# Kernel tuning notes

Hardware: AMD Instinct MI355X
Metric: run time of the kernel (lower is better)

The kernel has to match this reference:

```python
import jax, jax.numpy as jnp
import numpy as np

B, S, V, E, H, L = 64, 512, 32000, 512, 1024, 2


def setup_inputs() -> dict:
    key = jax.random.key(0)
    ks = jax.random.split(key, 12)
    sc = 0.05
    x = jax.random.randint(ks[0], (B, S), 0, V)
    emb = jax.random.normal(ks[1], (V, E), dtype=jnp.float32) * sc
    # Gate weights stacked along output dim in order [f, i, g, o] -> [4H, in_dim]
    Wx0 = jax.random.normal(ks[2], (4 * H, E), dtype=jnp.float32) * sc
    bx0 = jnp.zeros((4 * H,), dtype=jnp.float32)
    Wh0 = jax.random.normal(ks[3], (4 * H, H), dtype=jnp.float32) * sc
    bh0 = jnp.zeros((4 * H,), dtype=jnp.float32)
    Wx1 = jax.random.normal(ks[4], (4 * H, H), dtype=jnp.float32) * sc
    bx1 = jnp.zeros((4 * H,), dtype=jnp.float32)
    Wh1 = jax.random.normal(ks[5], (4 * H, H), dtype=jnp.float32) * sc
    bh1 = jnp.zeros((4 * H,), dtype=jnp.float32)
    fc_w = jax.random.normal(ks[6], (1, H), dtype=jnp.float32) * sc
    fc_b = jnp.zeros((1,), dtype=jnp.float32)
    return {"x": x, "emb": emb, "Wx0": Wx0, "bx0": bx0, "Wh0": Wh0, "bh0": bh0,
            "Wx1": Wx1, "bx1": bx1, "Wh1": Wh1, "bh1": bh1,
            "fc_w": fc_w, "fc_b": fc_b}


def _lstm_cell(inp, h, c, Wx, bx, Wh, bh):
    # Fused 4-gate GEMM, then split: order [forget, input, candidate, output]
    z = inp @ Wx.T + bx + h @ Wh.T + bh            # [B, 4H]
    f, i, g, o = jnp.split(z, 4, axis=-1)
    f = jax.nn.sigmoid(f)
    i = jax.nn.sigmoid(i)
    g = jnp.tanh(g)
    o = jax.nn.sigmoid(o)
    c = f * c + i * g
    h = o * jnp.tanh(c)
    return h, c


def reference(x, emb, Wx0, bx0, Wh0, bh0, Wx1, bx1, Wh1, bh1, fc_w, fc_b):
    xe = emb[x]                                     # [B, S, E]
    xts = jnp.swapaxes(xe, 0, 1)                    # [S, B, E] for scan
    b = xe.shape[0]
    zeros = jnp.zeros((b, H), dtype=xe.dtype)
    carry0 = (zeros, zeros, zeros, zeros)           # h0, c0, h1, c1

    def step(carry, xt):
        h0, c0, h1, c1 = carry
        h0, c0 = _lstm_cell(xt, h0, c0, Wx0, bx0, Wh0, bh0)
        h1, c1 = _lstm_cell(h0, h1, c1, Wx1, bx1, Wh1, bh1)
        return (h0, c0, h1, c1), None

    (h0, c0, h1, c1), _ = jax.lax.scan(step, carry0, xts)
    out = jax.nn.sigmoid(h1 @ fc_w.T + fc_b)        # [B, 1]
    return out
```

## Files before the change

kernel.cpp:

```cpp
#include <hip/hip_runtime.h>

#define BATCH 64
#define SLEN  512
#define EDIM  512
#define HDIM  1024
#define NBLK  256
#define HALF  128
#define K0    (EDIM + HDIM)
#define K1    (2 * HDIM)
#define ZR    32
#define ZST   68
#define HSLOT 65536
#define XROWB 512
#define RING  8

#define XE_BYTES ((size_t)SLEN * BATCH * XROWB)
#define HBUF_BIG ((size_t)SLEN * HSLOT)
#define HBUF_SML ((size_t)RING * HSLOT)

typedef _Float16 f16x8 __attribute__((ext_vector_type(8)));
typedef float  f32x4  __attribute__((ext_vector_type(4)));
typedef unsigned u32x4 __attribute__((ext_vector_type(4)));
typedef unsigned u32x2 __attribute__((ext_vector_type(2)));

__device__ __forceinline__ float sigm(float x) { return 1.0f / (1.0f + __expf(-x)); }
__device__ __forceinline__ float tanhfast(float x) {
  float e = __expf(-2.0f * __builtin_fabsf(x));
  float r = (1.0f - e) / (1.0f + e);
  return x < 0.0f ? -r : r;
}

__device__ __forceinline__ unsigned enc_e5m2(float v) {
  unsigned short hb = __builtin_bit_cast(unsigned short, (_Float16)v);
  return ((unsigned)hb + 0x80u) >> 8;
}

__device__ __forceinline__ void dec4(unsigned w, unsigned &lo, unsigned &hi) {
  lo = __builtin_amdgcn_perm(w, 0u, 0x05000400u);
  hi = __builtin_amdgcn_perm(w, 0u, 0x07000600u);
}

__device__ __forceinline__ void dec16(u32x4 d, f16x8 &fa, f16x8 &fb) {
  union { unsigned u[4]; f16x8 v; } A, B;
  dec4(d[0], A.u[0], A.u[1]); dec4(d[1], A.u[2], A.u[3]);
  dec4(d[2], B.u[0], B.u[1]); dec4(d[3], B.u[2], B.u[3]);
  fa = A.v; fb = B.v;
}

__device__ __forceinline__ void st8_wt(unsigned char* p, unsigned d0, unsigned d1) {
  u32x2 v = {d0, d1};
  asm volatile("global_store_dwordx2 %0, %1, off sc0 sc1" :: "v"(p), "v"(v) : "memory");
}

__device__ __forceinline__ u32x4 ald16b(const unsigned char* p) {
  union { unsigned long long q[2]; u32x4 v; } u;
  u.q[0] = __hip_atomic_load((const unsigned long long*)p,       __ATOMIC_RELAXED, __HIP_MEMORY_SCOPE_AGENT);
  u.q[1] = __hip_atomic_load((const unsigned long long*)(p + 8), __ATOMIC_RELAXED, __HIP_MEMORY_SCOPE_AGENT);
  return u.v;
}
template<int BIG>
__device__ __forceinline__ u32x4 hload16(const unsigned char* p) {
  if constexpr (BIG) return *(const u32x4*)p;
  else return ald16b(p);
}

__device__ __forceinline__ void block_wait(const int* f, int target, int* gate) {
  if (target <= 0) return;
  if ((threadIdx.x >> 6) == 0) {
    if (__hip_atomic_load(gate, __ATOMIC_RELAXED, __HIP_MEMORY_SCOPE_WORKGROUP) < target) {
      const int l = threadIdx.x & 63;
      int tries = 0;
      while (true) {
        int v0 = __hip_atomic_load(f + l,      __ATOMIC_RELAXED, __HIP_MEMORY_SCOPE_AGENT);
        int v1 = __hip_atomic_load(f + l + 64, __ATOMIC_RELAXED, __HIP_MEMORY_SCOPE_AGENT);
        if (__all((v0 >= target) && (v1 >= target))) break;
        __builtin_amdgcn_s_sleep(1);
        if (++tries > (1 << 21)) break;
      }
      if (l == 0)
        __hip_atomic_fetch_max(gate, target, __ATOMIC_RELEASE, __HIP_MEMORY_SCOPE_WORKGROUP);
    }
  } else {
    int tries = 0;
    while (__hip_atomic_load(gate, __ATOMIC_ACQUIRE, __HIP_MEMORY_SCOPE_WORKGROUP) < target) {
      __builtin_amdgcn_s_sleep(1);
      if (++tries > (1 << 21)) break;
    }
  }
}

__global__ void xe_gather(const int* __restrict__ x, const float* __restrict__ emb,
                          unsigned char* __restrict__ xe) {
  int g = blockIdx.x * blockDim.x + threadIdx.x;
  if (g >= SLEN * BATCH * (EDIM / 8)) return;
  int e8 = g & 63, bt = g >> 6;
  int b = bt & 63, t = bt >> 6;
  int tok = x[b * SLEN + t];
  const float* er = emb + (size_t)tok * EDIM + e8 * 8;
  f32x4 v0 = *(const f32x4*)er, v1 = *(const f32x4*)(er + 4);
  unsigned d0 = enc_e5m2(v0[0]) | (enc_e5m2(v0[1]) << 8) | (enc_e5m2(v0[2]) << 16) | (enc_e5m2(v0[3]) << 24);
  unsigned d1 = enc_e5m2(v1[0]) | (enc_e5m2(v1[1]) << 8) | (enc_e5m2(v1[2]) << 16) | (enc_e5m2(v1[3]) << 24);
  int pb = (e8 >> 3) * 64 + (e8 & 3) * 16 + ((e8 >> 2) & 1) * 8;
  *(u32x2*)(xe + ((size_t)t * BATCH + b) * XROWB + pb) = (u32x2){d0, d1};
}

#define MFMA(a, b, c) __builtin_amdgcn_mfma_f32_16x16x32_f16(a, b, c, 0, 0, 0)
#define LDSBF(t, kg) (*(const f16x8*)(&Ws[(size_t)((((t) * 64 + (kg)) * 64 + lane)) * 16]))

template<int BIG>
__global__ __launch_bounds__(512, 2) void lstm_persistent(
    const int* __restrict__ x, const float* __restrict__ emb,
    const float* __restrict__ Wx0, const float* __restrict__ bx0,
    const float* __restrict__ Wh0, const float* __restrict__ bh0,
    const float* __restrict__ Wx1, const float* __restrict__ bx1,
    const float* __restrict__ Wh1, const float* __restrict__ bh1,
    const unsigned char* __restrict__ xe, int use_xe,
    unsigned char* h0buf, unsigned char* h1buf, int* f0, int* f1)
{
  __shared__ __align__(16) unsigned char Ws[2 * 64 * 64 * 16];
  __shared__ float zbuf[BATCH * ZST];
  __shared__ float bias[ZR];
  __shared__ int gateF0, gateF1;

  const int tid   = threadIdx.x;
  const int wg    = blockIdx.x;
  const int layer = wg >> 7;
  const int sub   = wg & (HALF - 1);

  if (tid == 0) { gateF0 = 0; gateF1 = 0; }

  {
    const int KG = layer ? 64 : 48;
    for (int idx = tid; idx < 2 * KG * 64; idx += 512) {
      int t  = idx / (KG * 64);
      int r  = idx - t * (KG * 64);
      int kg = r >> 6, ln = r & 63;
      int n  = t * 16 + (ln & 15);
      int grow = (n >> 3) * HDIM + sub * 8 + (n & 7);
      int k  = kg * 32 + (ln >> 4) * 8;
      const float* src;
      if (layer == 0) src = (k < EDIM) ? (Wx0 + (size_t)grow * EDIM + k)
                                       : (Wh0 + (size_t)grow * HDIM + (k - EDIM));
      else            src = (k < HDIM) ? (Wx1 + (size_t)grow * HDIM + k)
                                       : (Wh1 + (size_t)grow * HDIM + (k - HDIM));
      f32x4 v0 = *(const f32x4*)src, v1 = *(const f32x4*)(src + 4);
      f16x8 o = { (_Float16)v0[0], (_Float16)v0[1], (_Float16)v0[2], (_Float16)v0[3],
                  (_Float16)v1[0], (_Float16)v1[1], (_Float16)v1[2], (_Float16)v1[3] };
      *(f16x8*)(&Ws[(size_t)((t * 64 + kg) * 64 + ln) * 16]) = o;
    }
    if (tid < ZR) {
      int grow = (tid >> 3) * HDIM + sub * 8 + (tid & 7);
      bias[tid] = layer ? (bx1[grow] + bh1[grow]) : (bx0[grow] + bh0[grow]);
    }
  }
  __syncthreads();

  const int lane = tid & 63, wave = tid >> 6;
  const int mrow = lane & 15;
  const int q    = lane >> 4;
  const int mt   = wave >> 1, nt = wave & 1;
  const int brow = mt * 16 + mrow;
  const int bg = tid >> 3, jl = tid & 7;
  const int zrow = mt * 16 + q * 4;
  const int pbase = (sub >> 3) * 64 + (sub & 3) * 16 + ((sub >> 2) & 1) * 8;

  float cst = 0.0f;

#define SLOTB(s) ((size_t)(BIG ? (s) : ((s) & (RING - 1))) * HSLOT)

#define ZWRITE()                                                                  \
  do {                                                                            \
    _Pragma("unroll")                                                             \
    for (int r = 0; r < 4; ++r) {                                                 \
      zbuf[(zrow + r) * ZST + nt * 34 + mrow]      = acc0[r];                     \
      zbuf[(zrow + r) * ZST + nt * 34 + 16 + mrow] = acc1[r];                     \
    }                                                                             \
  } while (0)

#define EPILOGUE(hdst, slotExpr)                                                  \
  do {                                                                            \
    float zf = zbuf[bg*ZST +      jl] + zbuf[bg*ZST + 34 +      jl] + bias[     jl]; \
    float zi = zbuf[bg*ZST +  8 + jl] + zbuf[bg*ZST + 34 +  8 + jl] + bias[ 8 + jl]; \
    float zg = zbuf[bg*ZST + 16 + jl] + zbuf[bg*ZST + 34 + 16 + jl] + bias[16 + jl]; \
    float zo = zbuf[bg*ZST + 24 + jl] + zbuf[bg*ZST + 34 + 24 + jl] + bias[24 + jl]; \
    float fg = sigm(zf), ig = sigm(zi), gg = tanhfast(zg), og = sigm(zo);         \
    cst = fg * cst + ig * gg;                                                     \
    unsigned by = enc_e5m2(og * tanhfast(cst));                                   \
    unsigned w0 = by | (((unsigned)__shfl_xor((int)by, 1, 64) & 0xFFu) << 8);     \
    w0 |= ((unsigned)__shfl_xor((int)w0, 2, 64) & 0xFFFFu) << 16;                 \
    unsigned dd1 = (unsigned)__shfl_xor((int)w0, 4, 64);                          \
    if (jl == 0)                                                                  \
      st8_wt(hdst + (slotExpr) + (size_t)bg * 1024 + pbase, w0, dd1);             \
    asm volatile("s_waitcnt vmcnt(0)" ::: "memory");                              \
  } while (0)

  if (layer == 0) {
    for (int s = 0; s < SLEN; ++s) {
      f32x4 acc0 = {0.f,0.f,0.f,0.f}, acc1 = {0.f,0.f,0.f,0.f};
      if (use_xe) {
        const unsigned char* aX = xe + ((size_t)s * BATCH + brow) * XROWB + nt * 256 + q * 16;
        #pragma unroll
        for (int g = 0; g < 4; ++g) {
          f16x8 fa, fb; dec16(*(const u32x4*)(aX + g * 64), fa, fb);
          const int kg = nt * 8 + g * 2;
          acc0 = MFMA(fa, LDSBF(0, kg), acc0);     acc1 = MFMA(fa, LDSBF(1, kg), acc1);
          acc0 = MFMA(fb, LDSBF(0, kg + 1), acc0); acc1 = MFMA(fb, LDSBF(1, kg + 1), acc1);
        }
      } else {
        const int tok = x[brow * SLEN + s];
        const float* erow = emb + (size_t)tok * EDIM;
        #pragma unroll
        for (int g = 0; g < 4; ++g) {
          const int k = nt * 256 + g * 64;
          const int kg = nt * 8 + g * 2;
          f32x4 e0 = *(const f32x4*)(erow + k + q * 8);
          f32x4 e1 = *(const f32x4*)(erow + k + q * 8 + 4);
          f16x8 fa = { (_Float16)e0[0], (_Float16)e0[1], (_Float16)e0[2], (_Float16)e0[3],
                       (_Float16)e1[0], (_Float16)e1[1], (_Float16)e1[2], (_Float16)e1[3] };
          f32x4 e2 = *(const f32x4*)(erow + k + 32 + q * 8);
          f32x4 e3 = *(const f32x4*)(erow + k + 32 + q * 8 + 4);
          f16x8 fb = { (_Float16)e2[0], (_Float16)e2[1], (_Float16)e2[2], (_Float16)e2[3],
                       (_Float16)e3[0], (_Float16)e3[1], (_Float16)e3[2], (_Float16)e3[3] };
          acc0 = MFMA(fa, LDSBF(0, kg), acc0);     acc1 = MFMA(fa, LDSBF(1, kg), acc1);
          acc0 = MFMA(fb, LDSBF(0, kg + 1), acc0); acc1 = MFMA(fb, LDSBF(1, kg + 1), acc1);
        }
      }
      if (s > 0) {
        block_wait(f0, s, &gateF0);
        const unsigned char* hp = h0buf + SLOTB(s - 1) + (size_t)brow * 1024 + nt * 512 + q * 16;
        #pragma unroll
        for (int g = 0; g < 8; ++g) {
          f16x8 fa, fb; dec16(hload16<BIG>(hp + g * 64), fa, fb);
          const int kg = 16 + nt * 16 + g * 2;
          acc0 = MFMA(fa, LDSBF(0, kg), acc0);     acc1 = MFMA(fa, LDSBF(1, kg), acc1);
          acc0 = MFMA(fb, LDSBF(0, kg + 1), acc0); acc1 = MFMA(fb, LDSBF(1, kg + 1), acc1);
        }
      }
      ZWRITE();
      __syncthreads();
      if constexpr (!BIG) {
        if (s >= RING) { block_wait(f1, s - RING + 2, &gateF1); block_wait(f0, s - RING + 2, &gateF0); }
      }
      EPILOGUE(h0buf, SLOTB(s));
      __syncthreads();
      if (tid == 0)
        __hip_atomic_store(&f0[sub], s + 1, __ATOMIC_RELAXED, __HIP_MEMORY_SCOPE_AGENT);
    }
  } else {
    for (int j = 0; j < SLEN; ++j) {
      f32x4 acc0 = {0.f,0.f,0.f,0.f}, acc1 = {0.f,0.f,0.f,0.f};
      block_wait(f0, j + 1, &gateF0);
      {
        const unsigned char* hp = h0buf + SLOTB(j) + (size_t)brow * 1024 + nt * 512 + q * 16;
        #pragma unroll
        for (int g = 0; g < 8; ++g) {
          f16x8 fa, fb; dec16(hload16<BIG>(hp + g * 64), fa, fb);
          const int kg = nt * 16 + g * 2;
          acc0 = MFMA(fa, LDSBF(0, kg), acc0);     acc1 = MFMA(fa, LDSBF(1, kg), acc1);
          acc0 = MFMA(fb, LDSBF(0, kg + 1), acc0); acc1 = MFMA(fb, LDSBF(1, kg + 1), acc1);
        }
      }
      if (j > 0) {
        block_wait(f1, j, &gateF1);
        const unsigned char* hp = h1buf + SLOTB(j - 1) + (size_t)brow * 1024 + nt * 512 + q * 16;
        #pragma unroll
        for (int g = 0; g < 8; ++g) {
          f16x8 fa, fb; dec16(hload16<BIG>(hp + g * 64), fa, fb);
          const int kg = 32 + nt * 16 + g * 2;
          acc0 = MFMA(fa, LDSBF(0, kg), acc0);     acc1 = MFMA(fa, LDSBF(1, kg), acc1);
          acc0 = MFMA(fb, LDSBF(0, kg + 1), acc0); acc1 = MFMA(fb, LDSBF(1, kg + 1), acc1);
        }
      }
      ZWRITE();
      __syncthreads();
      if constexpr (!BIG) {
        if (j >= RING) block_wait(f1, j - RING + 2, &gateF1);
      }
      EPILOGUE(h1buf, SLOTB(j));
      __syncthreads();
      if (tid == 0)
        __hip_atomic_store(&f1[sub], j + 1, __ATOMIC_RELAXED, __HIP_MEMORY_SCOPE_AGENT);
    }
  }
}

__global__ void fc_kernel(const unsigned char* __restrict__ h1slot,
                          const float* __restrict__ fcw, const float* __restrict__ fcb,
                          float* __restrict__ out) {
  __shared__ float part[512];
  const int tid = threadIdx.x, b = tid >> 3, q2 = tid & 7;
  const unsigned char* hr = h1slot + (size_t)b * 1024;
  float acc = 0.0f;
  for (int gg = 0; gg < 2; ++gg) {
    int g = q2 * 2 + gg;
    #pragma unroll
    for (int p = 0; p < 64; ++p) {
      unsigned by = hr[g * 64 + p];
      float hv = (float)__builtin_bit_cast(_Float16, (unsigned short)(by << 8));
      int qq = (p >> 4) & 3, hf = (p >> 3) & 1, jj = p & 7;
      acc += hv * fcw[g * 64 + hf * 32 + qq * 8 + jj];
    }
  }
  part[tid] = acc;
  __syncthreads();
  if (tid < BATCH) {
    float s = fcb[0];
    #pragma unroll
    for (int i = 0; i < 8; ++i) s += part[tid * 8 + i];
    out[tid] = 1.0f / (1.0f + __expf(-s));
  }
}

extern "C" void kernel_launch(void* const* d_in, const int* in_sizes, int n_in,
                              void* d_out, int out_size, void* d_ws, size_t ws_size,
                              hipStream_t stream) {
  (void)in_sizes; (void)n_in; (void)out_size;
  const int*   x   = (const int*)  d_in[0];
  const float* emb = (const float*)d_in[1];
  const float* Wx0 = (const float*)d_in[2];
  const float* bx0 = (const float*)d_in[3];
  const float* Wh0 = (const float*)d_in[4];
  const float* bh0 = (const float*)d_in[5];
  const float* Wx1 = (const float*)d_in[6];
  const float* bx1 = (const float*)d_in[7];
  const float* Wh1 = (const float*)d_in[8];
  const float* bh1 = (const float*)d_in[9];
  const float* fcw = (const float*)d_in[10];
  const float* fcb = (const float*)d_in[11];
  float* out = (float*)d_out;

  char* ws = (char*)d_ws;
  int* f0 = (int*)(ws);
  int* f1 = (int*)(ws + 512);

  const size_t need_big = 4096 + 2 * HBUF_BIG + XE_BYTES;
  const size_t need_sml = 4096 + 2 * HBUF_SML + XE_BYTES;
  const int big    = (ws_size >= need_big) ? 1 : 0;
  const size_t hbytes = big ? HBUF_BIG : HBUF_SML;
  unsigned char* h0buf = (unsigned char*)(ws + 4096);
  unsigned char* h1buf = (unsigned char*)(ws + 4096 + hbytes);
  unsigned char* xe    = (unsigned char*)(ws + 4096 + 2 * hbytes);
  const int use_xe = (big || ws_size >= need_sml) ? 1 : 0;

  hipMemsetAsync(d_ws, 0, 4096, stream);
  if (use_xe) {
    const int groups = SLEN * BATCH * (EDIM / 8);
    xe_gather<<<(groups + 255) / 256, 256, 0, stream>>>(x, emb, xe);
  }
  if (big) {
    lstm_persistent<1><<<NBLK, 512, 0, stream>>>(x, emb, Wx0, bx0, Wh0, bh0,
                                                 Wx1, bx1, Wh1, bh1,
                                                 xe, use_xe, h0buf, h1buf, f0, f1);
    fc_kernel<<<1, 512, 0, stream>>>(h1buf + (size_t)(SLEN - 1) * HSLOT, fcw, fcb, out);
  } else {
    lstm_persistent<0><<<NBLK, 512, 0, stream>>>(x, emb, Wx0, bx0, Wh0, bh0,
                                                 Wx1, bx1, Wh1, bh1,
                                                 xe, use_xe, h0buf, h1buf, f0, f1);
    fc_kernel<<<1, 512, 0, stream>>>(h1buf + (size_t)((SLEN - 1) & (RING - 1)) * HSLOT, fcw, fcb, out);
  }
}
```

Baseline: 2.892 ms.

## Specialize waves by input source and poll flags per wave

Splits K-dimension work across waves by source rather than halving it: in layer 0, waves 0-3 handle the embedding input while waves 4-7 handle the recurrent h; in layer 1, one group takes h0 and the other h1. Each wave now polls the cross-block flags directly instead of wave 0 polling and relaying through an LDS gate. The input-projection waves no longer wait on the recurrent dependency, so they can run ahead of it. The cost is uneven work per wave (512 vs 1024 K in layer 0) and more global polling traffic.

```diff
diff --git a/kernel.cpp b/kernel.cpp
--- a/kernel.cpp
+++ b/kernel.cpp
@@ -6,8 +6,6 @@
 #define HDIM  1024
 #define NBLK  256
 #define HALF  128
-#define K0    (EDIM + HDIM)
-#define K1    (2 * HDIM)
 #define ZR    32
 #define ZST   68
 #define HSLOT 65536
@@ -64,28 +62,16 @@
   else return ald16b(p);
 }
 
-__device__ __forceinline__ void block_wait(const int* f, int target, int* gate) {
+__device__ __forceinline__ void wave_wait(const int* f, int target) {
   if (target <= 0) return;
-  if ((threadIdx.x >> 6) == 0) {
-    if (__hip_atomic_load(gate, __ATOMIC_RELAXED, __HIP_MEMORY_SCOPE_WORKGROUP) < target) {
-      const int l = threadIdx.x & 63;
-      int tries = 0;
-      while (true) {
-        int v0 = __hip_atomic_load(f + l,      __ATOMIC_RELAXED, __HIP_MEMORY_SCOPE_AGENT);
-        int v1 = __hip_atomic_load(f + l + 64, __ATOMIC_RELAXED, __HIP_MEMORY_SCOPE_AGENT);
-        if (__all((v0 >= target) && (v1 >= target))) break;
-        __builtin_amdgcn_s_sleep(1);
-        if (++tries > (1 << 21)) break;
-      }
-      if (l == 0)
-        __hip_atomic_fetch_max(gate, target, __ATOMIC_RELEASE, __HIP_MEMORY_SCOPE_WORKGROUP);
-    }
-  } else {
-    int tries = 0;
-    while (__hip_atomic_load(gate, __ATOMIC_ACQUIRE, __HIP_MEMORY_SCOPE_WORKGROUP) < target) {
-      __builtin_amdgcn_s_sleep(1);
-      if (++tries > (1 << 21)) break;
-    }
+  const int l = threadIdx.x & 63;
+  int tries = 0;
+  while (true) {
+    int v0 = __hip_atomic_load(f + l,      __ATOMIC_RELAXED, __HIP_MEMORY_SCOPE_AGENT);
+    int v1 = __hip_atomic_load(f + l + 64, __ATOMIC_RELAXED, __HIP_MEMORY_SCOPE_AGENT);
+    if (__all((v0 >= target) && (v1 >= target))) return;
+    __builtin_amdgcn_s_sleep(1);
+    if (++tries > (1 << 21)) return;
   }
 }
 
@@ -120,14 +106,11 @@
   __shared__ __align__(16) unsigned char Ws[2 * 64 * 64 * 16];
   __shared__ float zbuf[BATCH * ZST];
   __shared__ float bias[ZR];
-  __shared__ int gateF0, gateF1;
 
   const int tid   = threadIdx.x;
   const int wg    = blockIdx.x;
   const int layer = wg >> 7;
   const int sub   = wg & (HALF - 1);
-
-  if (tid == 0) { gateF0 = 0; gateF1 = 0; }
 
   {
     const int KG = layer ? 64 : 48;
@@ -158,7 +141,8 @@
   const int lane = tid & 63, wave = tid >> 6;
   const int mrow = lane & 15;
   const int q    = lane >> 4;
-  const int mt   = wave >> 1, nt = wave & 1;
+  const int mt   = wave & 3;
+  const int spec = wave >> 2;
   const int brow = mt * 16 + mrow;
   const int bg = tid >> 3, jl = tid & 7;
   const int zrow = mt * 16 + q * 4;
@@ -172,8 +156,8 @@
   do {                                                                            \
     _Pragma("unroll")                                                             \
     for (int r = 0; r < 4; ++r) {                                                 \
-      zbuf[(zrow + r) * ZST + nt * 34 + mrow]      = acc0[r];                     \
-      zbuf[(zrow + r) * ZST + nt * 34 + 16 + mrow] = acc1[r];                     \
+      zbuf[(zrow + r) * ZST + spec * 34 + mrow]      = acc0[r];                   \
+      zbuf[(zrow + r) * ZST + spec * 34 + 16 + mrow] = acc1[r];                   \
     }                                                                             \
   } while (0)
 
@@ -194,52 +178,58 @@
     asm volatile("s_waitcnt vmcnt(0)" ::: "memory");                              \
   } while (0)
 
+#define HPART(hp, kgbase)                                                         \
+  do {                                                                            \
+    _Pragma("unroll")                                                             \
+    for (int g = 0; g < 16; ++g) {                                                \
+      f16x8 fa, fb; dec16(hload16<BIG>((hp) + g * 64), fa, fb);                   \
+      const int kg = (kgbase) + g * 2;                                            \
+      acc0 = MFMA(fa, LDSBF(0, kg), acc0);     acc1 = MFMA(fa, LDSBF(1, kg), acc1); \
+      acc0 = MFMA(fb, LDSBF(0, kg + 1), acc0); acc1 = MFMA(fb, LDSBF(1, kg + 1), acc1); \
+    }                                                                             \
+  } while (0)
+
   if (layer == 0) {
     for (int s = 0; s < SLEN; ++s) {
       f32x4 acc0 = {0.f,0.f,0.f,0.f}, acc1 = {0.f,0.f,0.f,0.f};
-      if (use_xe) {
-        const unsigned char* aX = xe + ((size_t)s * BATCH + brow) * XROWB + nt * 256 + q * 16;
-        #pragma unroll
-        for (int g = 0; g < 4; ++g) {
-          f16x8 fa, fb; dec16(*(const u32x4*)(aX + g * 64), fa, fb);
-          const int kg = nt * 8 + g * 2;
-          acc0 = MFMA(fa, LDSBF(0, kg), acc0);     acc1 = MFMA(fa, LDSBF(1, kg), acc1);
-          acc0 = MFMA(fb, LDSBF(0, kg + 1), acc0); acc1 = MFMA(fb, LDSBF(1, kg + 1), acc1);
+      if (spec == 0) {
+        if (use_xe) {
+          const unsigned char* aX = xe + ((size_t)s * BATCH + brow) * XROWB + q * 16;
+          #pragma unroll
+          for (int g = 0; g < 8; ++g) {
+            f16x8 fa, fb; dec16(*(const u32x4*)(aX + g * 64), fa, fb);
+            const int kg = g * 2;
+            acc0 = MFMA(fa, LDSBF(0, kg), acc0);     acc1 = MFMA(fa, LDSBF(1, kg), acc1);
+            acc0 = MFMA(fb, LDSBF(0, kg + 1), acc0); acc1 = MFMA(fb, LDSBF(1, kg + 1), acc1);
+          }
+        } else {
+          const int tok = x[brow * SLEN + s];
+          const float* erow = emb + (size_t)tok * EDIM;
+          #pragma unroll
+          for (int g = 0; g < 8; ++g) {
+            const int k = g * 64;
+            f32x4 e0 = *(const f32x4*)(erow + k + q * 8);
+            f32x4 e1 = *(const f32x4*)(erow + k + q * 8 + 4);
+            f16x8 fa = { (_Float16)e0[0], (_Float16)e0[1], (_Float16)e0[2], (_Float16)e0[3],
+                         (_Float16)e1[0], (_Float16)e1[1], (_Float16)e1[2], (_Float16)e1[3] };
+            f32x4 e2 = *(const f32x4*)(erow + k + 32 + q * 8);
+            f32x4 e3 = *(const f32x4*)(erow + k + 32 + q * 8 + 4);
+            f16x8 fb = { (_Float16)e2[0], (_Float16)e2[1], (_Float16)e2[2], (_Float16)e2[3],
+                         (_Float16)e3[0], (_Float16)e3[1], (_Float16)e3[2], (_Float16)e3[3] };
+            const int kg = g * 2;
+            acc0 = MFMA(fa, LDSBF(0, kg), acc0);     acc1 = MFMA(fa, LDSBF(1, kg), acc1);
+            acc0 = MFMA(fb, LDSBF(0, kg + 1), acc0); acc1 = MFMA(fb, LDSBF(1, kg + 1), acc1);
+          }
         }
-      } else {
-        const int tok = x[brow * SLEN + s];
-        const float* erow = emb + (size_t)tok * EDIM;
-        #pragma unroll
-        for (int g = 0; g < 4; ++g) {
-          const int k = nt * 256 + g * 64;
-          const int kg = nt * 8 + g * 2;
-          f32x4 e0 = *(const f32x4*)(erow + k + q * 8);
-          f32x4 e1 = *(const f32x4*)(erow + k + q * 8 + 4);
-          f16x8 fa = { (_Float16)e0[0], (_Float16)e0[1], (_Float16)e0[2], (_Float16)e0[3],
-                       (_Float16)e1[0], (_Float16)e1[1], (_Float16)e1[2], (_Float16)e1[3] };
-          f32x4 e2 = *(const f32x4*)(erow + k + 32 + q * 8);
-          f32x4 e3 = *(const f32x4*)(erow + k + 32 + q * 8 + 4);
-          f16x8 fb = { (_Float16)e2[0], (_Float16)e2[1], (_Float16)e2[2], (_Float16)e2[3],
-                       (_Float16)e3[0], (_Float16)e3[1], (_Float16)e3[2], (_Float16)e3[3] };
-          acc0 = MFMA(fa, LDSBF(0, kg), acc0);     acc1 = MFMA(fa, LDSBF(1, kg), acc1);
-          acc0 = MFMA(fb, LDSBF(0, kg + 1), acc0); acc1 = MFMA(fb, LDSBF(1, kg + 1), acc1);
-        }
-      }
-      if (s > 0) {
-        block_wait(f0, s, &gateF0);
-        const unsigned char* hp = h0buf + SLOTB(s - 1) + (size_t)brow * 1024 + nt * 512 + q * 16;
-        #pragma unroll
-        for (int g = 0; g < 8; ++g) {
-          f16x8 fa, fb; dec16(hload16<BIG>(hp + g * 64), fa, fb);
-          const int kg = 16 + nt * 16 + g * 2;
-          acc0 = MFMA(fa, LDSBF(0, kg), acc0);     acc1 = MFMA(fa, LDSBF(1, kg), acc1);
-          acc0 = MFMA(fb, LDSBF(0, kg + 1), acc0); acc1 = MFMA(fb, LDSBF(1, kg + 1), acc1);
-        }
+      } else if (s > 0) {
+        wave_wait(f0, s);
+        const unsigned char* hp = h0buf + SLOTB(s - 1) + (size_t)brow * 1024 + q * 16;
+        HPART(hp, 16);
       }
       ZWRITE();
       __syncthreads();
       if constexpr (!BIG) {
-        if (s >= RING) { block_wait(f1, s - RING + 2, &gateF1); block_wait(f0, s - RING + 2, &gateF0); }
+        if (s >= RING) { wave_wait(f1, s - RING + 2); wave_wait(f0, s - RING + 2); }
       }
       EPILOGUE(h0buf, SLOTB(s));
       __syncthreads();
@@ -249,32 +239,19 @@
   } else {
     for (int j = 0; j < SLEN; ++j) {
       f32x4 acc0 = {0.f,0.f,0.f,0.f}, acc1 = {0.f,0.f,0.f,0.f};
-      block_wait(f0, j + 1, &gateF0);
-      {
-        const unsigned char* hp = h0buf + SLOTB(j) + (size_t)brow * 1024 + nt * 512 + q * 16;
-        #pragma unroll
-        for (int g = 0; g < 8; ++g) {
-          f16x8 fa, fb; dec16(hload16<BIG>(hp + g * 64), fa, fb);
-          const int kg = nt * 16 + g * 2;
-          acc0 = MFMA(fa, LDSBF(0, kg), acc0);     acc1 = MFMA(fa, LDSBF(1, kg), acc1);
-          acc0 = MFMA(fb, LDSBF(0, kg + 1), acc0); acc1 = MFMA(fb, LDSBF(1, kg + 1), acc1);
-        }
-      }
-      if (j > 0) {
-        block_wait(f1, j, &gateF1);
-        const unsigned char* hp = h1buf + SLOTB(j - 1) + (size_t)brow * 1024 + nt * 512 + q * 16;
-        #pragma unroll
-        for (int g = 0; g < 8; ++g) {
-          f16x8 fa, fb; dec16(hload16<BIG>(hp + g * 64), fa, fb);
-          const int kg = 32 + nt * 16 + g * 2;
-          acc0 = MFMA(fa, LDSBF(0, kg), acc0);     acc1 = MFMA(fa, LDSBF(1, kg), acc1);
-          acc0 = MFMA(fb, LDSBF(0, kg + 1), acc0); acc1 = MFMA(fb, LDSBF(1, kg + 1), acc1);
-        }
+      if (spec == 0) {
+        wave_wait(f0, j + 1);
+        const unsigned char* hp = h0buf + SLOTB(j) + (size_t)brow * 1024 + q * 16;
+        HPART(hp, 0);
+      } else if (j > 0) {
+        wave_wait(f1, j);
+        const unsigned char* hp = h1buf + SLOTB(j - 1) + (size_t)brow * 1024 + q * 16;
+        HPART(hp, 32);
       }
       ZWRITE();
       __syncthreads();
       if constexpr (!BIG) {
-        if (j >= RING) block_wait(f1, j - RING + 2, &gateF1);
+        if (j >= RING) wave_wait(f1, j - RING + 2);
       }
       EPILOGUE(h1buf, SLOTB(j));
       __syncthreads();
```

Result: slower. 4.560 ms (+57.7%).
